# Optimization experiments

Hardware: AMD Instinct MI355X
Metric: run time of the kernel (lower is better)

Reference implementation:

```python
import jax, jax.numpy as jnp
import numpy as np

EMBED_DIM = 1024
NUM_HEADS = 16


def setup_inputs() -> dict:
    key = jax.random.key(0)
    k_x, k_w, k_b, k_ow, k_ob = jax.random.split(key, 5)
    B, S, E = 4, 2048, EMBED_DIM
    scale = 1.0 / np.sqrt(E)
    x = jax.random.normal(k_x, (B, S, E), dtype=jnp.float32)
    # nn.MultiheadAttention packed in-projection [3E, E] and out projection [E, E]
    in_proj_w = jax.random.uniform(k_w, (3 * E, E), dtype=jnp.float32, minval=-scale, maxval=scale)
    in_proj_b = jnp.zeros((3 * E,), dtype=jnp.float32)
    out_proj_w = jax.random.uniform(k_ow, (E, E), dtype=jnp.float32, minval=-scale, maxval=scale)
    out_proj_b = jnp.zeros((E,), dtype=jnp.float32)
    return {"x": x, "in_proj_w": in_proj_w, "in_proj_b": in_proj_b,
            "out_proj_w": out_proj_w, "out_proj_b": out_proj_b}


def reference(x, in_proj_w, in_proj_b, out_proj_w, out_proj_b):
    B, S, E = x.shape
    H = NUM_HEADS
    hd = E // H
    # packed QKV projection: [B,S,3E]
    qkv = x @ in_proj_w.T + in_proj_b
    q, k, v = jnp.split(qkv, 3, axis=-1)
    # [B,S,E] -> [B,H,S,hd]
    def to_heads(t):
        return t.reshape(B, S, H, hd).transpose(0, 2, 1, 3)
    q, k, v = to_heads(q), to_heads(k), to_heads(v)
    scale = 1.0 / jnp.sqrt(jnp.asarray(hd, dtype=x.dtype))
    scores = jnp.einsum('bhqd,bhkd->bhqk', q * scale, k)  # [B,H,S,S]
    # causal mask: position i attends to <= i (matches the -inf additive mask)
    causal = jnp.tril(jnp.ones((S, S), dtype=bool))
    scores = jnp.where(causal[None, None, :, :], scores, jnp.finfo(x.dtype).min)
    attn = jax.nn.softmax(scores, axis=-1)
    out = jnp.einsum('bhqk,bhkd->bhqd', attn, v)  # [B,H,S,hd]
    out = out.transpose(0, 2, 1, 3).reshape(B, S, E)
    return out @ out_proj_w.T + out_proj_b
```

## Files before the change

kernel.cpp:

```cpp
#include <hip/hip_runtime.h>
#include <stdint.h>

typedef _Float16 f16;
typedef _Float16 f16x2 __attribute__((ext_vector_type(2)));
typedef _Float16 f16x8 __attribute__((ext_vector_type(8)));
typedef float f32x4 __attribute__((ext_vector_type(4)));
typedef float f32x16 __attribute__((ext_vector_type(16)));
typedef uint32_t u32x4 __attribute__((ext_vector_type(4)));

#define B_   4
#define S_   2048
#define E_   1024
#define H_   16
#define HD_  64
#define BH_  (B_ * H_)

template <int N> struct IC { static constexpr int v = N; };

__device__ __forceinline__ void async_lds16(const void* g, void* l) {
    __builtin_amdgcn_global_load_lds(
        (__attribute__((address_space(1))) void*)(uintptr_t)g,
        (__attribute__((address_space(3))) void*)(uint32_t)(uintptr_t)l,
        16, 0, 0);
}

__global__ __launch_bounds__(256)
void cvt3(const float* __restrict__ x, const float* __restrict__ w1,
          const float* __restrict__ w2, f16* __restrict__ xb,
          f16* __restrict__ w1b, f16* __restrict__ w2b)
{
    const long i = (long)blockIdx.x * 256 + threadIdx.x;
    const float* src; f16* dst; long j;
    if (i < 1048576)      { src = x;  dst = xb;  j = i; }
    else if (i < 1441792) { src = w1; dst = w1b; j = i - 1048576; }
    else                  { src = w2; dst = w2b; j = i - 1441792; }
    const float4* p = (const float4*)src;
    float4 a = p[2 * j], b = p[2 * j + 1];
    f16x8 o;
    o[0] = (f16)a.x; o[1] = (f16)a.y; o[2] = (f16)a.z; o[3] = (f16)a.w;
    o[4] = (f16)b.x; o[5] = (f16)b.y; o[6] = (f16)b.z; o[7] = (f16)b.w;
    *(f16x8*)(dst + 8 * j) = o;
}

template <int MODE>
__global__ __launch_bounds__(512)
void gemm_pipe(const f16* __restrict__ A, const f16* __restrict__ Bm,
               const float* __restrict__ bias,
               f16* __restrict__ qo, f16* __restrict__ ko, f16* __restrict__ vto,
               float* __restrict__ Cf)
{
    constexpr int K = 1024, NT = 16;
    constexpr int N = (MODE == 0) ? 3072 : 1024;
    constexpr int NTN = N / 256;
    constexpr int NBLK = 64 * NTN;
    __shared__ __align__(16) f16 L[3][(128 + 256) * 64];
    const int tid = threadIdx.x, wave = tid >> 6, lane = tid & 63;
    const int lo = lane & 15, hi = lane >> 4;
    const int bid0 = blockIdx.x;
    const int bid = (bid0 & 7) * (NBLK / 8) + (bid0 >> 3);
    const int tm = bid / NTN, tn = bid % NTN;
    const long bm0 = (long)tm * 128, bn0 = (long)tn * 256;
    const int wr = (wave >> 2) * 64, wc = (wave & 3) * 64;

#define STAGE6(BUF, T)  do {                                                      \
    const long kk = (long)(T) * 64;                                               \
    _Pragma("unroll")                                                             \
    for (int j = 0; j < 2; ++j) {                                                 \
        const int c = j * 512 + tid;                                              \
        const int row = c >> 3, ch = c & 7;                                       \
        async_lds16(A + (bm0 + row) * K + kk + ((ch ^ (row & 7)) * 8),            \
                    &L[BUF][(j * 512 + wave * 64) * 8]);                          \
    }                                                                             \
    _Pragma("unroll")                                                             \
    for (int j = 0; j < 4; ++j) {                                                 \
        const int c = j * 512 + tid;                                              \
        const int row = c >> 3, ch = c & 7;                                       \
        async_lds16(Bm + (bn0 + row) * K + kk + ((ch ^ (row & 7)) * 8),           \
                    &L[BUF][8192 + (j * 512 + wave * 64) * 8]);                   \
    } } while (0)

    f32x4 acc[4][4] = {};

    auto tile = [&](auto bufc, int t) {
        constexpr int BUF = decltype(bufc)::v;
        constexpr int SBUF = (BUF + 2) % 3;
        if (t + 2 < NT) STAGE6(SBUF, t + 2);
        f16x8 af[2][4], bf[2][4];
#pragma unroll
        for (int kh = 0; kh < 2; ++kh) {
#pragma unroll
            for (int mi = 0; mi < 4; ++mi) {
                const int r = wr + mi * 16 + lo;
                af[kh][mi] = *(const f16x8*)&L[BUF][(r * 8 + ((kh * 4 + hi) ^ (r & 7))) * 8];
            }
#pragma unroll
            for (int ni = 0; ni < 4; ++ni) {
                const int r = wc + ni * 16 + lo;
                bf[kh][ni] = *(const f16x8*)&L[BUF][8192 + (r * 8 + ((kh * 4 + hi) ^ (r & 7))) * 8];
            }
        }
        __builtin_amdgcn_s_setprio(1);
#pragma unroll
        for (int kh = 0; kh < 2; ++kh)
#pragma unroll
            for (int mi = 0; mi < 4; ++mi)
#pragma unroll
                for (int ni = 0; ni < 4; ++ni)
                    acc[mi][ni] = __builtin_amdgcn_mfma_f32_16x16x32_f16(
                        af[kh][mi], bf[kh][ni], acc[mi][ni], 0, 0, 0);
        __builtin_amdgcn_s_setprio(0);
        if (t + 2 < NT) asm volatile("s_waitcnt vmcnt(6)" ::: "memory");
        else            asm volatile("s_waitcnt vmcnt(0)" ::: "memory");
        __builtin_amdgcn_sched_barrier(0);
        __builtin_amdgcn_s_barrier();
    };

    STAGE6(0, 0);
    STAGE6(1, 1);
    asm volatile("s_waitcnt vmcnt(6)" ::: "memory");
    __builtin_amdgcn_sched_barrier(0);
    __builtin_amdgcn_s_barrier();
    for (int t = 0; t < 15; t += 3) {
        tile(IC<0>{}, t);
        tile(IC<1>{}, t + 1);
        tile(IC<2>{}, t + 2);
    }
    tile(IC<0>{}, 15);
#undef STAGE6

    if (MODE == 1) {
#pragma unroll
        for (int mi = 0; mi < 4; ++mi)
#pragma unroll
            for (int ni = 0; ni < 4; ++ni)
#pragma unroll
                for (int j = 0; j < 4; ++j) {
                    const long r  = bm0 + wr + mi * 16 + 4 * hi + j;
                    const int  cn = (int)bn0 + wc + ni * 16 + lo;
                    Cf[r * N + cn] = acc[mi][ni][j] + bias[cn];
                }
        return;
    }

    const int which = (int)(bn0 >> 10);
    if (which < 2) {
#pragma unroll
        for (int mi = 0; mi < 4; ++mi)
#pragma unroll
            for (int ni = 0; ni < 4; ++ni)
#pragma unroll
                for (int j = 0; j < 4; ++j) {
                    const long r  = bm0 + wr + mi * 16 + 4 * hi + j;
                    const int  cn = (int)bn0 + wc + ni * 16 + lo;
                    const int  e = cn & 1023, h = e >> 6, d = e & 63;
                    const int  b = (int)(r >> 11), s = (int)(r & 2047);
                    const long bh = (long)b * H_ + h;
                    const f16 hv = (f16)(acc[mi][ni][j] + bias[cn]);
                    if (which == 0) qo[(bh * S_ + s) * HD_ + d] = hv;
                    else            ko[(bh * S_ + s) * HD_ + d] = hv;
                }
    } else {
        f16* T = ((f16*)L) + wave * 4096;
#pragma unroll
        for (int ni = 0; ni < 4; ++ni) {
            const int dl = ni * 16 + lo;
            const int dx = dl & 7;
#pragma unroll
            for (int mi = 0; mi < 4; ++mi)
#pragma unroll
                for (int j = 0; j < 4; ++j) {
                    const int sl = mi * 16 + 4 * hi + j;
                    const int cn = (int)bn0 + wc + ni * 16 + lo;
                    T[dl * 64 + ((((sl >> 3) ^ dx) << 3) | (sl & 7))] =
                        (f16)(acc[mi][ni][j] + bias[cn]);
                }
        }
        const int b = (int)(bm0 >> 11);
        const int sbase = (int)(bm0 & 2047) + wr;
        const int h = ((int)(bn0 & 1023) + wc) >> 6;
        const long vbase = (long)(b * H_ + h) * HD_;
#pragma unroll
        for (int it = 0; it < 8; ++it) {
            const int d = it * 8 + (lane >> 3);
            const int schunk = lane & 7;
            u32x4 val = *(const u32x4*)&T[d * 64 + ((schunk ^ (d & 7)) << 3)];
            *(u32x4*)&vto[(vbase + d) * S_ + sbase + schunk * 8] = val;
        }
    }
}

__global__ __launch_bounds__(256)
void attn_fwd(const f16* __restrict__ qb, const f16* __restrict__ kb,
              const f16* __restrict__ vtb, f16* __restrict__ ob)
{
    __shared__ __align__(16) f16 Ks[2][64 * 64];
    __shared__ __align__(16) f16 Vs[2][64 * 64];
    const int tid = threadIdx.x, wave = tid >> 6, lane = tid & 63;
    const int q32 = lane & 31, h2 = lane >> 5;
    const int bh = blockIdx.x;
    const int qtA = blockIdx.y;
    const int qtB = 15 - qtA;
    const int qwA = qtA * 128 + wave * 32;
    const int qwB = qtB * 128 + wave * 32;
    const long krow0 = (long)bh * S_;
    const long vrow0 = (long)bh * HD_;

#define STAGE(BUF, KV)  do {                                                      \
    _Pragma("unroll")                                                             \
    for (int p = 0; p < 2; ++p) {                                                 \
        const int n = p * 256 + tid;                                              \
        const int base = (p * 256 + wave * 64) * 8;                               \
        async_lds16(kb  + (krow0 + (KV) + (n & 63)) * HD_ + (n >> 6) * 8, &Ks[BUF][base]); \
        async_lds16(vtb + (vrow0 + (n & 63)) * S_ + (KV) + (n >> 6) * 8, &Vs[BUF][base]);  \
    } } while (0)

    f16x8 qfA[4], qfB[4];
    const f16 sch = (f16)0.1803368801f;
#pragma unroll
    for (int kkq = 0; kkq < 4; ++kkq) {
        qfA[kkq] = *(const f16x8*)&qb[(krow0 + qwA + q32) * HD_ + kkq * 16 + h2 * 8];
        qfB[kkq] = *(const f16x8*)&qb[(krow0 + qwB + q32) * HD_ + kkq * 16 + h2 * 8];
#pragma unroll
        for (int e = 0; e < 8; ++e) { qfA[kkq][e] *= sch; qfB[kkq][e] *= sch; }
    }

    f32x16 oaccA[2] = {}, oaccB[2] = {};
    float lA = 0.f, lB = 0.f;
    const f16x2 ones2 = { (f16)1.0f, (f16)1.0f };

    auto computeS = [&](auto bufc, auto spc, int t) {
        constexpr int BUF = decltype(bufc)::v;
        constexpr int SP  = decltype(spc)::v;
        const int qw = SP ? qwB : qwA;
        const f16x8* qf = SP ? qfB : qfA;
        f32x16* oacc = SP ? oaccB : oaccA;
        float& l_part = SP ? lB : lA;
        const int kv0 = t * 64;
        if (kv0 > qw + 31) return;
        const int qg = qw + q32;

        f32x16 sc[2] = {};
        __builtin_amdgcn_s_setprio(1);
#pragma unroll
        for (int kkq = 0; kkq < 4; ++kkq)
#pragma unroll
            for (int ni = 0; ni < 2; ++ni) {
                f16x8 kf = *(const f16x8*)&Ks[BUF][(((kkq * 2 + h2) * 64) + ni * 32 + q32) * 8];
                sc[ni] = __builtin_amdgcn_mfma_f32_32x32x16_f16(kf, qf[kkq], sc[ni], 0, 0, 0);
            }
        __builtin_amdgcn_s_setprio(0);

        const bool maskp = (kv0 + 63) > qw;
#pragma unroll
        for (int ni = 0; ni < 2; ++ni)
#pragma unroll
            for (int r = 0; r < 16; ++r) {
                float p = __builtin_amdgcn_exp2f(sc[ni][r]);
                const int kvg = kv0 + ni * 32 + (r & 3) + 8 * (r >> 2) + 4 * h2;
                if (maskp && kvg > qg) p = 0.0f;
                sc[ni][r] = p;
            }

        __builtin_amdgcn_s_setprio(1);
#pragma unroll
        for (int ni = 0; ni < 2; ++ni) {
            uint32_t u[8];
#pragma unroll
            for (int m = 0; m < 8; ++m) {
                auto hp = __builtin_amdgcn_cvt_pkrtz(sc[ni][2 * m], sc[ni][2 * m + 1]);
                u[m] = __builtin_bit_cast(uint32_t, hp);
                l_part = __builtin_amdgcn_fdot2(__builtin_bit_cast(f16x2, u[m]), ones2, l_part, false);
            }
#pragma unroll
            for (int kkv = 0; kkv < 2; ++kkv) {
                auto sA = __builtin_amdgcn_permlane32_swap(u[4 * kkv + 0], u[4 * kkv + 2], false, false);
                auto sB = __builtin_amdgcn_permlane32_swap(u[4 * kkv + 1], u[4 * kkv + 3], false, false);
                u32x4 uv = { (uint32_t)sA[0], (uint32_t)sB[0], (uint32_t)sA[1], (uint32_t)sB[1] };
                f16x8 pf = __builtin_bit_cast(f16x8, uv);
                const int kg = ni * 2 + kkv;
#pragma unroll
                for (int dh = 0; dh < 2; ++dh) {
                    f16x8 vf = *(const f16x8*)&Vs[BUF][(((kg * 2 + h2) * 64) + dh * 32 + q32) * 8];
                    oacc[dh] = __builtin_amdgcn_mfma_f32_32x32x16_f16(pf, vf, oacc[dh], 0, 0, 0);
                }
            }
        }
        __builtin_amdgcn_s_setprio(0);
    };

    const int ntB = 2 * (qtB + 1);
    STAGE(0, 0);
    __syncthreads();
    for (int t = 0; t < ntB; t += 2) {
        STAGE(1, (t + 1) * 64);
        computeS(IC<0>{}, IC<0>{}, t);
        computeS(IC<0>{}, IC<1>{}, t);
        __syncthreads();
        if (t + 2 < ntB) STAGE(0, (t + 2) * 64);
        computeS(IC<1>{}, IC<0>{}, t + 1);
        computeS(IC<1>{}, IC<1>{}, t + 1);
        __syncthreads();
    }
#undef STAGE

    const int b = bh >> 4, h = bh & 15;
    const float invA = 1.0f / (lA + __shfl_xor(lA, 32));
    const float invB = 1.0f / (lB + __shfl_xor(lB, 32));
#pragma unroll
    for (int r = 0; r < 16; ++r) {
        const int crow = (r & 3) + 8 * (r >> 2) + 4 * h2;
        const float irA = __shfl(invA, crow);
        const float irB = __shfl(invB, crow);
#pragma unroll
        for (int dh = 0; dh < 2; ++dh) {
            ob[((long)b * S_ + qwA + crow) * E_ + h * HD_ + dh * 32 + q32] = (f16)(oaccA[dh][r] * irA);
            ob[((long)b * S_ + qwB + crow) * E_ + h * HD_ + dh * 32 + q32] = (f16)(oaccB[dh][r] * irB);
        }
    }
}

extern "C" void kernel_launch(void* const* d_in, const int* in_sizes, int n_in,
                              void* d_out, int out_size, void* d_ws, size_t ws_size,
                              hipStream_t stream)
{
    (void)in_sizes; (void)n_in; (void)out_size; (void)ws_size;
    const float* x  = (const float*)d_in[0];
    const float* w1 = (const float*)d_in[1];
    const float* b1 = (const float*)d_in[2];
    const float* w2 = (const float*)d_in[3];
    const float* b2 = (const float*)d_in[4];
    float* out = (float*)d_out;

    char* ws = (char*)d_ws;
    f16* xb  = (f16*)ws;  ws += (size_t)8192 * 1024 * 2;
    f16* w1b = (f16*)ws;  ws += (size_t)3072 * 1024 * 2;
    f16* w2b = (f16*)ws;  ws += (size_t)1024 * 1024 * 2;
    f16* qb  = (f16*)ws;  ws += (size_t)BH_ * S_ * HD_ * 2;
    f16* kb  = (f16*)ws;  ws += (size_t)BH_ * S_ * HD_ * 2;
    f16* vtb = (f16*)ws;  ws += (size_t)BH_ * S_ * HD_ * 2;
    f16* ao  = (f16*)ws;  ws += (size_t)8192 * 1024 * 2;

    cvt3<<<dim3(6144), dim3(256), 0, stream>>>(x, w1, w2, xb, w1b, w2b);

    gemm_pipe<0><<<dim3(768), dim3(512), 0, stream>>>(xb, w1b, b1, qb, kb, vtb, nullptr);

    attn_fwd<<<dim3(64, 8), dim3(256), 0, stream>>>(qb, kb, vtb, ao);

    gemm_pipe<1><<<dim3(256), dim3(512), 0, stream>>>(ao, w2b, b2, nullptr, nullptr, nullptr, out);
}
```

Measured before the change: 148.8 us.

## Interleave both query sub-tiles per KV block and compute row sums via MFMA

Merges the two per-sub-tile attention passes into one lambda that issues QK and PV MFMAs for both query strips together, sharing each K/V fragment load and giving the scheduler independent MFMA chains to interleave. The softmax denominator is no longer accumulated with fdot2 plus cross-lane shuffles. It now comes from an extra MFMA of P against a ones matrix, so it lands in the same accumulator layout as the output. This removes the final shuffles and the fdot2 VALU work, at the cost of extra MFMA issues and higher register pressure from the doubled live accumulators.

Measured after the change: 175.3 us. 1.18x slower.

```diff
diff --git a/kernel.cpp b/kernel.cpp
--- a/kernel.cpp
+++ b/kernel.cpp
@@ -224,64 +224,90 @@
         for (int e = 0; e < 8; ++e) { qfA[kkq][e] *= sch; qfB[kkq][e] *= sch; }
     }
 
+    f16x8 ones8;
+#pragma unroll
+    for (int e = 0; e < 8; ++e) ones8[e] = (f16)1.0f;
+
     f32x16 oaccA[2] = {}, oaccB[2] = {};
-    float lA = 0.f, lB = 0.f;
-    const f16x2 ones2 = { (f16)1.0f, (f16)1.0f };
-
-    auto computeS = [&](auto bufc, auto spc, int t) {
-        constexpr int BUF = decltype(bufc)::v;
-        constexpr int SP  = decltype(spc)::v;
-        const int qw = SP ? qwB : qwA;
-        const f16x8* qf = SP ? qfB : qfA;
-        f32x16* oacc = SP ? oaccB : oaccA;
-        float& l_part = SP ? lB : lA;
+    f32x16 laccA = {}, laccB = {};
+
+    auto compute = [&](auto bufc, auto actc, int t) {
+        constexpr int BUF  = decltype(bufc)::v;
+        constexpr int ACTA = decltype(actc)::v;
         const int kv0 = t * 64;
-        if (kv0 > qw + 31) return;
-        const int qg = qw + q32;
-
-        f32x16 sc[2] = {};
+
+        f32x16 scA[2] = {}, scB[2] = {};
         __builtin_amdgcn_s_setprio(1);
 #pragma unroll
         for (int kkq = 0; kkq < 4; ++kkq)
 #pragma unroll
             for (int ni = 0; ni < 2; ++ni) {
                 f16x8 kf = *(const f16x8*)&Ks[BUF][(((kkq * 2 + h2) * 64) + ni * 32 + q32) * 8];
-                sc[ni] = __builtin_amdgcn_mfma_f32_32x32x16_f16(kf, qf[kkq], sc[ni], 0, 0, 0);
+                scB[ni] = __builtin_amdgcn_mfma_f32_32x32x16_f16(kf, qfB[kkq], scB[ni], 0, 0, 0);
+                if constexpr (ACTA)
+                    scA[ni] = __builtin_amdgcn_mfma_f32_32x32x16_f16(kf, qfA[kkq], scA[ni], 0, 0, 0);
             }
         __builtin_amdgcn_s_setprio(0);
 
-        const bool maskp = (kv0 + 63) > qw;
+        const bool maskB = (kv0 + 63) > qwB;
+        const int qgB = qwB + q32;
 #pragma unroll
         for (int ni = 0; ni < 2; ++ni)
 #pragma unroll
             for (int r = 0; r < 16; ++r) {
-                float p = __builtin_amdgcn_exp2f(sc[ni][r]);
+                float p = __builtin_amdgcn_exp2f(scB[ni][r]);
                 const int kvg = kv0 + ni * 32 + (r & 3) + 8 * (r >> 2) + 4 * h2;
-                if (maskp && kvg > qg) p = 0.0f;
-                sc[ni][r] = p;
-            }
+                if (maskB && kvg > qgB) p = 0.0f;
+                scB[ni][r] = p;
+            }
+        if constexpr (ACTA) {
+            const bool maskA = (kv0 + 63) > qwA;
+            const int qgA = qwA + q32;
+#pragma unroll
+            for (int ni = 0; ni < 2; ++ni)
+#pragma unroll
+                for (int r = 0; r < 16; ++r) {
+                    float p = __builtin_amdgcn_exp2f(scA[ni][r]);
+                    const int kvg = kv0 + ni * 32 + (r & 3) + 8 * (r >> 2) + 4 * h2;
+                    if (maskA && kvg > qgA) p = 0.0f;
+                    scA[ni][r] = p;
+                }
+        }
 
         __builtin_amdgcn_s_setprio(1);
 #pragma unroll
         for (int ni = 0; ni < 2; ++ni) {
-            uint32_t u[8];
+            uint32_t uB[8], uA[8];
 #pragma unroll
             for (int m = 0; m < 8; ++m) {
-                auto hp = __builtin_amdgcn_cvt_pkrtz(sc[ni][2 * m], sc[ni][2 * m + 1]);
-                u[m] = __builtin_bit_cast(uint32_t, hp);
-                l_part = __builtin_amdgcn_fdot2(__builtin_bit_cast(f16x2, u[m]), ones2, l_part, false);
+                uB[m] = __builtin_bit_cast(uint32_t,
+                        __builtin_amdgcn_cvt_pkrtz(scB[ni][2 * m], scB[ni][2 * m + 1]));
+                if constexpr (ACTA)
+                    uA[m] = __builtin_bit_cast(uint32_t,
+                            __builtin_amdgcn_cvt_pkrtz(scA[ni][2 * m], scA[ni][2 * m + 1]));
             }
 #pragma unroll
             for (int kkv = 0; kkv < 2; ++kkv) {
-                auto sA = __builtin_amdgcn_permlane32_swap(u[4 * kkv + 0], u[4 * kkv + 2], false, false);
-                auto sB = __builtin_amdgcn_permlane32_swap(u[4 * kkv + 1], u[4 * kkv + 3], false, false);
-                u32x4 uv = { (uint32_t)sA[0], (uint32_t)sB[0], (uint32_t)sA[1], (uint32_t)sB[1] };
-                f16x8 pf = __builtin_bit_cast(f16x8, uv);
+                auto sA1 = __builtin_amdgcn_permlane32_swap(uB[4 * kkv + 0], uB[4 * kkv + 2], false, false);
+                auto sB1 = __builtin_amdgcn_permlane32_swap(uB[4 * kkv + 1], uB[4 * kkv + 3], false, false);
+                u32x4 uvB = { (uint32_t)sA1[0], (uint32_t)sB1[0], (uint32_t)sA1[1], (uint32_t)sB1[1] };
+                f16x8 pfB = __builtin_bit_cast(f16x8, uvB);
+                laccB = __builtin_amdgcn_mfma_f32_32x32x16_f16(pfB, ones8, laccB, 0, 0, 0);
+                f16x8 pfA;
+                if constexpr (ACTA) {
+                    auto sA2 = __builtin_amdgcn_permlane32_swap(uA[4 * kkv + 0], uA[4 * kkv + 2], false, false);
+                    auto sB2 = __builtin_amdgcn_permlane32_swap(uA[4 * kkv + 1], uA[4 * kkv + 3], false, false);
+                    u32x4 uvA = { (uint32_t)sA2[0], (uint32_t)sB2[0], (uint32_t)sA2[1], (uint32_t)sB2[1] };
+                    pfA = __builtin_bit_cast(f16x8, uvA);
+                    laccA = __builtin_amdgcn_mfma_f32_32x32x16_f16(pfA, ones8, laccA, 0, 0, 0);
+                }
                 const int kg = ni * 2 + kkv;
 #pragma unroll
                 for (int dh = 0; dh < 2; ++dh) {
                     f16x8 vf = *(const f16x8*)&Vs[BUF][(((kg * 2 + h2) * 64) + dh * 32 + q32) * 8];
-                    oacc[dh] = __builtin_amdgcn_mfma_f32_32x32x16_f16(pf, vf, oacc[dh], 0, 0, 0);
+                    oaccB[dh] = __builtin_amdgcn_mfma_f32_32x32x16_f16(pfB, vf, oaccB[dh], 0, 0, 0);
+                    if constexpr (ACTA)
+                        oaccA[dh] = __builtin_amdgcn_mfma_f32_32x32x16_f16(pfA, vf, oaccA[dh], 0, 0, 0);
                 }
             }
         }
@@ -293,24 +319,22 @@
     __syncthreads();
     for (int t = 0; t < ntB; t += 2) {
         STAGE(1, (t + 1) * 64);
-        computeS(IC<0>{}, IC<0>{}, t);
-        computeS(IC<0>{}, IC<1>{}, t);
+        if (t * 64 <= qwA + 31) compute(IC<0>{}, IC<1>{}, t);
+        else                    compute(IC<0>{}, IC<0>{}, t);
         __syncthreads();
         if (t + 2 < ntB) STAGE(0, (t + 2) * 64);
-        computeS(IC<1>{}, IC<0>{}, t + 1);
-        computeS(IC<1>{}, IC<1>{}, t + 1);
+        if ((t + 1) * 64 <= qwA + 31) compute(IC<1>{}, IC<1>{}, t + 1);
+        else                          compute(IC<1>{}, IC<0>{}, t + 1);
         __syncthreads();
     }
 #undef STAGE
 
     const int b = bh >> 4, h = bh & 15;
-    const float invA = 1.0f / (lA + __shfl_xor(lA, 32));
-    const float invB = 1.0f / (lB + __shfl_xor(lB, 32));
 #pragma unroll
     for (int r = 0; r < 16; ++r) {
         const int crow = (r & 3) + 8 * (r >> 2) + 4 * h2;
-        const float irA = __shfl(invA, crow);
-        const float irB = __shfl(invB, crow);
+        const float irA = 1.0f / laccA[r];
+        const float irB = 1.0f / laccB[r];
 #pragma unroll
         for (int dh = 0; dh < 2; ++dh) {
             ob[((long)b * S_ + qwA + crow) * E_ + h * HD_ + dh * 32 + q32] = (f16)(oaccA[dh][r] * irA);
```

## Split attention query strips across 8 waves instead of 2 strips per wave

Applied to the files above, without the earlier changes.

The attention block now launches 512 threads (8 waves). Each wave owns a single 32-row query slab from either the low or the high paired tile, instead of each of 4 waves processing both. The wave-to-strip mapping is interleaved so the causal workload stays balanced across SIMDs. This halves per-wave registers and MFMA serial work and lets staging use one load per thread, at the cost of more waves contending for LDS and barriers, and idle waves on the short strip.

Measured after the change: 159.5 us. 1.07x slower.

```diff
diff --git a/kernel.cpp b/kernel.cpp
--- a/kernel.cpp
+++ b/kernel.cpp
@@ -189,7 +189,7 @@
     }
 }
 
-__global__ __launch_bounds__(256)
+__global__ __launch_bounds__(512)
 void attn_fwd(const f16* __restrict__ qb, const f16* __restrict__ kb,
               const f16* __restrict__ vtb, f16* __restrict__ ob)
 {
@@ -200,44 +200,37 @@
     const int bh = blockIdx.x;
     const int qtA = blockIdx.y;
     const int qtB = 15 - qtA;
-    const int qwA = qtA * 128 + wave * 32;
-    const int qwB = qtB * 128 + wave * 32;
+    const int strip = (wave ^ (wave >> 2)) & 1;
+    const int wrow  = wave >> 1;
+    const int qw = (strip ? qtB : qtA) * 128 + wrow * 32;
     const long krow0 = (long)bh * S_;
     const long vrow0 = (long)bh * HD_;
 
 #define STAGE(BUF, KV)  do {                                                      \
-    _Pragma("unroll")                                                             \
-    for (int p = 0; p < 2; ++p) {                                                 \
-        const int n = p * 256 + tid;                                              \
-        const int base = (p * 256 + wave * 64) * 8;                               \
-        async_lds16(kb  + (krow0 + (KV) + (n & 63)) * HD_ + (n >> 6) * 8, &Ks[BUF][base]); \
-        async_lds16(vtb + (vrow0 + (n & 63)) * S_ + (KV) + (n >> 6) * 8, &Vs[BUF][base]);  \
-    } } while (0)
-
-    f16x8 qfA[4], qfB[4];
+    async_lds16(kb  + (krow0 + (KV) + (tid & 63)) * HD_ + (tid >> 6) * 8,         \
+                &Ks[BUF][wave * 512]);                                            \
+    async_lds16(vtb + (vrow0 + (tid & 63)) * S_ + (KV) + (tid >> 6) * 8,          \
+                &Vs[BUF][wave * 512]);                                            \
+    } while (0)
+
+    f16x8 qf[4];
     const f16 sch = (f16)0.1803368801f;
 #pragma unroll
     for (int kkq = 0; kkq < 4; ++kkq) {
-        qfA[kkq] = *(const f16x8*)&qb[(krow0 + qwA + q32) * HD_ + kkq * 16 + h2 * 8];
-        qfB[kkq] = *(const f16x8*)&qb[(krow0 + qwB + q32) * HD_ + kkq * 16 + h2 * 8];
-#pragma unroll
-        for (int e = 0; e < 8; ++e) { qfA[kkq][e] *= sch; qfB[kkq][e] *= sch; }
-    }
-
-    f32x16 oaccA[2] = {}, oaccB[2] = {};
-    float lA = 0.f, lB = 0.f;
+        qf[kkq] = *(const f16x8*)&qb[(krow0 + qw + q32) * HD_ + kkq * 16 + h2 * 8];
+#pragma unroll
+        for (int e = 0; e < 8; ++e) qf[kkq][e] *= sch;
+    }
+
+    f32x16 oacc[2] = {};
+    float l_part = 0.f;
     const f16x2 ones2 = { (f16)1.0f, (f16)1.0f };
-
-    auto computeS = [&](auto bufc, auto spc, int t) {
+    const int qg = qw + q32;
+
+    auto compute = [&](auto bufc, int t) {
         constexpr int BUF = decltype(bufc)::v;
-        constexpr int SP  = decltype(spc)::v;
-        const int qw = SP ? qwB : qwA;
-        const f16x8* qf = SP ? qfB : qfA;
-        f32x16* oacc = SP ? oaccB : oaccA;
-        float& l_part = SP ? lB : lA;
         const int kv0 = t * 64;
         if (kv0 > qw + 31) return;
-        const int qg = qw + q32;
 
         f32x16 sc[2] = {};
         __builtin_amdgcn_s_setprio(1);
@@ -293,29 +286,23 @@
     __syncthreads();
     for (int t = 0; t < ntB; t += 2) {
         STAGE(1, (t + 1) * 64);
-        computeS(IC<0>{}, IC<0>{}, t);
-        computeS(IC<0>{}, IC<1>{}, t);
+        compute(IC<0>{}, t);
         __syncthreads();
         if (t + 2 < ntB) STAGE(0, (t + 2) * 64);
-        computeS(IC<1>{}, IC<0>{}, t + 1);
-        computeS(IC<1>{}, IC<1>{}, t + 1);
+        compute(IC<1>{}, t + 1);
         __syncthreads();
     }
 #undef STAGE
 
     const int b = bh >> 4, h = bh & 15;
-    const float invA = 1.0f / (lA + __shfl_xor(lA, 32));
-    const float invB = 1.0f / (lB + __shfl_xor(lB, 32));
+    const float inv = 1.0f / (l_part + __shfl_xor(l_part, 32));
 #pragma unroll
     for (int r = 0; r < 16; ++r) {
         const int crow = (r & 3) + 8 * (r >> 2) + 4 * h2;
-        const float irA = __shfl(invA, crow);
-        const float irB = __shfl(invB, crow);
-#pragma unroll
-        for (int dh = 0; dh < 2; ++dh) {
-            ob[((long)b * S_ + qwA + crow) * E_ + h * HD_ + dh * 32 + q32] = (f16)(oaccA[dh][r] * irA);
-            ob[((long)b * S_ + qwB + crow) * E_ + h * HD_ + dh * 32 + q32] = (f16)(oaccB[dh][r] * irB);
-        }
+        const float invr = __shfl(inv, crow);
+#pragma unroll
+        for (int dh = 0; dh < 2; ++dh)
+            ob[((long)b * S_ + qw + crow) * E_ + h * HD_ + dh * 32 + q32] = (f16)(oacc[dh][r] * invr);
     }
 }
 
@@ -344,7 +331,7 @@
 
     gemm_pipe<0><<<dim3(768), dim3(512), 0, stream>>>(xb, w1b, b1, qb, kb, vtb, nullptr);
 
-    attn_fwd<<<dim3(64, 8), dim3(256), 0, stream>>>(qb, kb, vtb, ao);
+    attn_fwd<<<dim3(64, 8), dim3(512), 0, stream>>>(qb, kb, vtb, ao);
 
     gemm_pipe<1><<<dim3(256), dim3(512), 0, stream>>>(ao, w2b, b2, nullptr, nullptr, nullptr, out);
 }
```

## Split attention KV range into two halves and combine with normalization kernel

Applied to the files above, without the earlier changes.

Each (batch-head, query-tile-pair) attention block is split along the key/value axis into two halves selected by blockIdx.y. This doubles the attention grid to improve occupancy and load balance. Each half writes unnormalized fp16 partial outputs and row sums into reused workspace buffers. A new elementwise kernel then adds the two partials and divides by the summed denominators. The trade-off is an extra kernel launch plus extra global memory traffic for the partials. Correctness relies on both halves sharing the same max reference, and unnormalized fp16 partials risk precision loss.

New measurement: 193.5 us. 1.3x slower.

```diff
diff --git a/kernel.cpp b/kernel.cpp
--- a/kernel.cpp
+++ b/kernel.cpp
@@ -191,14 +191,17 @@
 
 __global__ __launch_bounds__(256)
 void attn_fwd(const f16* __restrict__ qb, const f16* __restrict__ kb,
-              const f16* __restrict__ vtb, f16* __restrict__ ob)
+              const f16* __restrict__ vtb,
+              f16* __restrict__ po0, f16* __restrict__ po1,
+              float* __restrict__ pl0, float* __restrict__ pl1)
 {
     __shared__ __align__(16) f16 Ks[2][64 * 64];
     __shared__ __align__(16) f16 Vs[2][64 * 64];
     const int tid = threadIdx.x, wave = tid >> 6, lane = tid & 63;
     const int q32 = lane & 31, h2 = lane >> 5;
     const int bh = blockIdx.x;
-    const int qtA = blockIdx.y;
+    const int z   = blockIdx.y >> 3;
+    const int qtA = blockIdx.y & 7;
     const int qtB = 15 - qtA;
     const int qwA = qtA * 128 + wave * 32;
     const int qwB = qtB * 128 + wave * 32;
@@ -288,35 +291,62 @@
         __builtin_amdgcn_s_setprio(0);
     };
 
-    const int ntB = 2 * (qtB + 1);
-    STAGE(0, 0);
+    const int ntB  = 2 * (qtB + 1);
+    const int half = qtB + 1;
+    const int t0 = z ? half : 0;
+    const int t1 = z ? ntB  : half;
+
+    STAGE(0, t0 * 64);
     __syncthreads();
-    for (int t = 0; t < ntB; t += 2) {
-        STAGE(1, (t + 1) * 64);
+    for (int t = t0; t < t1; t += 2) {
+        if (t + 1 < t1) STAGE(1, (t + 1) * 64);
         computeS(IC<0>{}, IC<0>{}, t);
         computeS(IC<0>{}, IC<1>{}, t);
         __syncthreads();
-        if (t + 2 < ntB) STAGE(0, (t + 2) * 64);
-        computeS(IC<1>{}, IC<0>{}, t + 1);
-        computeS(IC<1>{}, IC<1>{}, t + 1);
+        if (t + 2 < t1) STAGE(0, (t + 2) * 64);
+        if (t + 1 < t1) {
+            computeS(IC<1>{}, IC<0>{}, t + 1);
+            computeS(IC<1>{}, IC<1>{}, t + 1);
+        }
         __syncthreads();
     }
 #undef STAGE
 
     const int b = bh >> 4, h = bh & 15;
-    const float invA = 1.0f / (lA + __shfl_xor(lA, 32));
-    const float invB = 1.0f / (lB + __shfl_xor(lB, 32));
+    f16* po = z ? po1 : po0;
+    float* pl = z ? pl1 : pl0;
+    const float ltA = lA + __shfl_xor(lA, 32);
+    const float ltB = lB + __shfl_xor(lB, 32);
+    if (h2 == 0) {
+        pl[((long)b * S_ + qwA + q32) * 16 + h] = ltA;
+        pl[((long)b * S_ + qwB + q32) * 16 + h] = ltB;
+    }
 #pragma unroll
     for (int r = 0; r < 16; ++r) {
         const int crow = (r & 3) + 8 * (r >> 2) + 4 * h2;
-        const float irA = __shfl(invA, crow);
-        const float irB = __shfl(invB, crow);
 #pragma unroll
         for (int dh = 0; dh < 2; ++dh) {
-            ob[((long)b * S_ + qwA + crow) * E_ + h * HD_ + dh * 32 + q32] = (f16)(oaccA[dh][r] * irA);
-            ob[((long)b * S_ + qwB + crow) * E_ + h * HD_ + dh * 32 + q32] = (f16)(oaccB[dh][r] * irB);
-        }
-    }
+            po[((long)b * S_ + qwA + crow) * E_ + h * HD_ + dh * 32 + q32] = (f16)oaccA[dh][r];
+            po[((long)b * S_ + qwB + crow) * E_ + h * HD_ + dh * 32 + q32] = (f16)oaccB[dh][r];
+        }
+    }
+}
+
+__global__ __launch_bounds__(256)
+void norm_combine(const f16* __restrict__ po0, const f16* __restrict__ po1,
+                  const float* __restrict__ pl0, const float* __restrict__ pl1,
+                  f16* __restrict__ ao)
+{
+    const long i = (long)blockIdx.x * 256 + threadIdx.x;
+    const long ridx = i >> 3;
+    const float inv = 1.0f / (pl0[ridx] + pl1[ridx]);
+    f16x8 a = *(const f16x8*)(po0 + 8 * i);
+    f16x8 b = *(const f16x8*)(po1 + 8 * i);
+    f16x8 o;
+#pragma unroll
+    for (int e = 0; e < 8; ++e)
+        o[e] = (f16)(((float)a[e] + (float)b[e]) * inv);
+    *(f16x8*)(ao + 8 * i) = o;
 }
 
 extern "C" void kernel_launch(void* const* d_in, const int* in_sizes, int n_in,
@@ -340,11 +370,18 @@
     f16* vtb = (f16*)ws;  ws += (size_t)BH_ * S_ * HD_ * 2;
     f16* ao  = (f16*)ws;  ws += (size_t)8192 * 1024 * 2;
 
+    f16*   po0 = xb;
+    f16*   po1 = (f16*)d_out;
+    float* pl0 = (float*)w1b;
+    float* pl1 = pl0 + (size_t)BH_ * S_;
+
     cvt3<<<dim3(6144), dim3(256), 0, stream>>>(x, w1, w2, xb, w1b, w2b);
 
     gemm_pipe<0><<<dim3(768), dim3(512), 0, stream>>>(xb, w1b, b1, qb, kb, vtb, nullptr);
 
-    attn_fwd<<<dim3(64, 8), dim3(256), 0, stream>>>(qb, kb, vtb, ao);
+    attn_fwd<<<dim3(64, 16), dim3(256), 0, stream>>>(qb, kb, vtb, po0, po1, pl0, pl1);
+
+    norm_combine<<<dim3(4096), dim3(256), 0, stream>>>(po0, po1, pl0, pl1, ao);
 
     gemm_pipe<1><<<dim3(256), dim3(512), 0, stream>>>(ao, w2b, b2, nullptr, nullptr, nullptr, out);
 }
```
